# Kernel optimization log

Hardware: AMD Instinct MI355X
Metric: run time of the kernel (lower is better)

The kernel has to match this reference:

```python
import jax, jax.numpy as jnp
import numpy as np

CHEB_K = 3


def setup_inputs() -> dict:
    key = jax.random.key(0)
    k1, k2, k3 = jax.random.split(key, 3)
    B, N, C = 64, 2048, 64
    E, O = 16, 64
    x = jax.random.normal(k1, (B, N, C), dtype=jnp.float32)
    node_embeddings = jax.random.normal(k2, (N, E), dtype=jnp.float32)
    # xavier-uniform-like init for weights_pool (embed_dim, cheb_k, dim_in, dim_out)
    fan_in, fan_out = E * CHEB_K * C, O
    limit = float(np.sqrt(6.0 / (fan_in + fan_out)))
    weights_pool = jax.random.uniform(k3, (E, CHEB_K, C, O), dtype=jnp.float32,
                                      minval=-limit, maxval=limit)
    bias_pool = jnp.zeros((E, O), dtype=jnp.float32)
    return {"x": x, "node_embeddings": node_embeddings,
            "weights_pool": weights_pool, "bias_pool": bias_pool}


def reference(x, node_embeddings, weights_pool, bias_pool):
    N = node_embeddings.shape[0]
    # adaptive adjacency: softmax(relu(E E^T)) row-wise   [N, N]
    supports = jax.nn.softmax(jax.nn.relu(node_embeddings @ node_embeddings.T), axis=1)
    # Chebyshev recurrence: T0 = I, T1 = A, Tk = 2*A*T_{k-1} - T_{k-2}
    support_set = [jnp.eye(N, dtype=supports.dtype), supports]
    for _ in range(2, CHEB_K):
        support_set.append(2.0 * supports @ support_set[-1] - support_set[-2])
    supports_k = jnp.stack(support_set, axis=0)  # [K, N, N]
    # per-node dynamic weights / bias from pools
    weights = jnp.einsum('nd,dkio->nkio', node_embeddings, weights_pool)  # [N,K,C,O]
    bias = node_embeddings @ bias_pool                                    # [N,O]
    # graph conv: gather Chebyshev features then per-node grouped GEMM
    x_g = jnp.einsum('knm,bmc->bnkc', supports_k, x)       # [B,N,K,C]
    x_gconv = jnp.einsum('bnki,nkio->bno', x_g, weights) + bias  # [B,N,O]
    return x_gconv
```

## Files before the change

### kernel.cpp

```cpp
#include <hip/hip_runtime.h>
#include <hip/hip_bf16.h>

#define BB 64
#define NN 2048
#define CC 64
#define EE 16
#define OO 64
#define JJ 4096

typedef __attribute__((ext_vector_type(8))) short short8;
typedef __attribute__((ext_vector_type(4))) float f32x4;
typedef __attribute__((ext_vector_type(4))) unsigned short u16x4;
typedef __attribute__((ext_vector_type(8))) unsigned short u16x8;

__device__ __forceinline__ unsigned short f2bf(float f) {
  __hip_bfloat16 h = __float2bfloat16(f);
  return *reinterpret_cast<unsigned short*>(&h);
}
__device__ __forceinline__ float bf2f(unsigned short u) {
  unsigned int v = ((unsigned int)u) << 16;
  return *reinterpret_cast<float*>(&v);
}
__device__ __forceinline__ void gload16(const void* g, void* l) {
  __builtin_amdgcn_global_load_lds(
      (const __attribute__((address_space(1))) unsigned int*)g,
      (__attribute__((address_space(3))) unsigned int*)l, 16, 0, 0);
}

__global__ __launch_bounds__(256) void supports_kernel(
    const float* __restrict__ emb, unsigned short* __restrict__ A)
{
  int n = blockIdx.x;
  int tid = threadIdx.x;
  float en[EE];
#pragma unroll
  for (int d = 0; d < EE; ++d) en[d] = emb[n*EE + d];

  float logit[8];
  float lmax = 0.0f;
#pragma unroll
  for (int i = 0; i < 8; ++i) {
    int m = i*256 + tid;
    const float* em = emb + m*EE;
    float s = 0.f;
#pragma unroll
    for (int d = 0; d < EE; ++d) s = fmaf(en[d], em[d], s);
    s = fmaxf(s, 0.f);
    logit[i] = s;
    lmax = fmaxf(lmax, s);
  }
  __shared__ float red[256];
  red[tid] = lmax; __syncthreads();
  for (int s = 128; s > 0; s >>= 1) {
    if (tid < s) red[tid] = fmaxf(red[tid], red[tid+s]);
    __syncthreads();
  }
  lmax = red[0]; __syncthreads();
  float sum = 0.f;
#pragma unroll
  for (int i = 0; i < 8; ++i) {
    float e = __expf(logit[i]-lmax);
    logit[i] = e; sum += e;
  }
  red[tid] = sum; __syncthreads();
  for (int s = 128; s > 0; s >>= 1) {
    if (tid < s) red[tid] += red[tid+s];
    __syncthreads();
  }
  float inv = 1.f/red[0];
#pragma unroll
  for (int i = 0; i < 8; ++i) A[(size_t)n*NN + i*256 + tid] = f2bf(logit[i]*inv);
}

__global__ __launch_bounds__(256) void xpose_kernel(
    const float* __restrict__ x, unsigned short* __restrict__ Xt)
{
  int b = blockIdx.y;
  int n0 = blockIdx.x * 64;
  __shared__ float T[64][65];
  int tid = threadIdx.x;
  int r = tid >> 4, c4 = (tid & 15) * 4;
  const float* src = x + ((size_t)b*NN + n0)*64;
#pragma unroll
  for (int rr = r; rr < 64; rr += 16) {
    float4 v = *(const float4*)(src + rr*64 + c4);
    T[rr][c4] = v.x; T[rr][c4+1] = v.y; T[rr][c4+2] = v.z; T[rr][c4+3] = v.w;
  }
  __syncthreads();
  int c = tid >> 2, q0 = (tid & 3) * 16;
  unsigned short* dst = Xt + ((size_t)b*64 + c)*NN + n0 + q0;
  u16x8 o0, o1;
#pragma unroll
  for (int q = 0; q < 8; ++q) o0[q] = f2bf(T[q0+q][c]);
#pragma unroll
  for (int q = 0; q < 8; ++q) o1[q] = f2bf(T[q0+8+q][c]);
  *(u16x8*)(dst) = o0;
  *(u16x8*)(dst + 8) = o1;
}

__device__ __forceinline__ void stage_tile(
    const unsigned short* __restrict__ A, const unsigned short* __restrict__ Bt,
    unsigned short* as, unsigned short* bs,
    int m0, int j0, int k0, int wid, int lrow, int lu)
{
#pragma unroll
  for (int li = 0; li < 4; ++li) {
    int rb = wid*32 + li*8;
    int r = rb + lrow;
    int su = lu ^ (r & 7);
    gload16(A  + (size_t)(m0 + r)*2048 + k0 + su*8, as + rb*64);
    gload16(Bt + (size_t)(j0 + r)*2048 + k0 + su*8, bs + rb*64);
  }
}

__global__ __launch_bounds__(256) void gemm_bt_bf16(
    const unsigned short* __restrict__ A, const unsigned short* __restrict__ Bt,
    unsigned short* __restrict__ Crow, unsigned short* __restrict__ Ct, int writeT)
{
  __shared__ unsigned short As[2][128*64];
  __shared__ unsigned short Bs[2][128*64];
  int tid = threadIdx.x;
  int bid = blockIdx.x;
  int swz = (bid & 7) * 64 + (bid >> 3);
  int m0 = (swz >> 5) * 128, j0 = (swz & 31) * 128;
  int wid = tid >> 6, lane = tid & 63;
  int wm = wid >> 1, wn = wid & 1;
  int fr = lane & 15, kg = lane >> 4;
  int lrow = lane >> 3, lu = lane & 7;

  f32x4 acc[4][4];
#pragma unroll
  for (int i = 0; i < 4; ++i)
#pragma unroll
    for (int j = 0; j < 4; ++j) acc[i][j] = (f32x4){0.f,0.f,0.f,0.f};

  stage_tile(A, Bt, As[0], Bs[0], m0, j0, 0, wid, lrow, lu);

  int cur = 0;
#pragma unroll 2
  for (int k0 = 0; k0 < 2048; k0 += 64) {
    if (k0 + 64 < 2048) {
      stage_tile(A, Bt, As[cur^1], Bs[cur^1], m0, j0, k0 + 64, wid, lrow, lu);
      asm volatile("s_waitcnt vmcnt(8)" ::: "memory");
    } else {
      asm volatile("s_waitcnt vmcnt(0)" ::: "memory");
    }
    __builtin_amdgcn_s_barrier();
    asm volatile("" ::: "memory");

    const unsigned short* asb = As[cur];
    const unsigned short* bsb = Bs[cur];
#pragma unroll
    for (int ks = 0; ks < 2; ++ks) {
      short8 af[4], bv[4];
#pragma unroll
      for (int i = 0; i < 4; ++i) {
        int r = wm*64 + i*16 + fr;
        int u = ((ks << 2) | kg) ^ (r & 7);
        af[i] = *(const short8*)((const char*)asb + r*128 + u*16);
      }
#pragma unroll
      for (int j = 0; j < 4; ++j) {
        int r = wn*64 + j*16 + fr;
        int u = ((ks << 2) | kg) ^ (r & 7);
        bv[j] = *(const short8*)((const char*)bsb + r*128 + u*16);
      }
#pragma unroll
      for (int i = 0; i < 4; ++i)
#pragma unroll
        for (int j = 0; j < 4; ++j)
          acc[i][j] = __builtin_amdgcn_mfma_f32_16x16x32_bf16(af[i], bv[j], acc[i][j], 0, 0, 0);
    }
    asm volatile("" ::: "memory");
    __builtin_amdgcn_s_barrier();
    cur ^= 1;
  }

  int mrow4 = (lane >> 4) * 4;
#pragma unroll
  for (int i = 0; i < 4; ++i) {
    int mbase = m0 + wm*64 + i*16 + mrow4;
#pragma unroll
    for (int j = 0; j < 4; ++j) {
      int jcol = j0 + wn*64 + j*16 + fr;
      f32x4 v = acc[i][j];
      if (writeT) {
        u16x4 pk = { f2bf(v[0]), f2bf(v[1]), f2bf(v[2]), f2bf(v[3]) };
        *(u16x4*)(Ct + (size_t)jcol*2048 + mbase) = pk;
      }
      Crow[(size_t)(mbase+0)*4096 + jcol] = f2bf(v[0]);
      Crow[(size_t)(mbase+1)*4096 + jcol] = f2bf(v[1]);
      Crow[(size_t)(mbase+2)*4096 + jcol] = f2bf(v[2]);
      Crow[(size_t)(mbase+3)*4096 + jcol] = f2bf(v[3]);
    }
  }
}

__global__ __launch_bounds__(256) void wgen_kernel(
    const float* __restrict__ emb, const float* __restrict__ wp,
    unsigned short* __restrict__ wtg)
{
  __shared__ unsigned short Wlds[8][64*72];
  __shared__ float e_s[8][16];
  int tid = threadIdx.x;
  int g = blockIdx.x, r = blockIdx.y;
  int n0 = g*8;
  if (tid < 128) e_s[tid >> 4][tid & 15] = emb[n0*16 + tid];
  __syncthreads();
  int o = tid & 63, w = tid >> 6;
#pragma unroll 1
  for (int p = 0; p < 2; ++p) {
    int u = r*8 + p*4 + w;
    float acc[8][8];
#pragma unroll
    for (int n = 0; n < 8; ++n)
#pragma unroll
      for (int q = 0; q < 8; ++q) acc[n][q] = 0.f;
    const float* wpp = wp + u*512 + o;
#pragma unroll
    for (int d = 0; d < 16; ++d) {
      float wv[8];
#pragma unroll
      for (int q = 0; q < 8; ++q) wv[q] = wpp[d*12288 + q*64];
#pragma unroll
      for (int n = 0; n < 8; ++n) {
        float en = e_s[n][d];
#pragma unroll
        for (int q = 0; q < 8; ++q) acc[n][q] = fmaf(en, wv[q], acc[n][q]);
      }
    }
    int slot = (u & 7) ^ (o & 7);
#pragma unroll
    for (int n = 0; n < 8; ++n) {
      u16x8 pk;
#pragma unroll
      for (int q = 0; q < 8; ++q) pk[q] = f2bf(acc[n][q]);
      *(u16x8*)&Wlds[n][o*72 + slot*8] = pk;
    }
  }
  __syncthreads();
#pragma unroll
  for (int half = 0; half < 2; ++half) {
    int nd = half*4 + (tid >> 6);
    unsigned short* dst = wtg + (size_t)(n0+nd)*12288 + o*192 + r*64;
#pragma unroll
    for (int s = 0; s < 8; ++s)
      *(u16x8*)(dst + s*8) = *(const u16x8*)&Wlds[nd][o*72 + s*8];
  }
}

#define FNPB 4
__global__ __launch_bounds__(256) void final_mfma(
    const float* __restrict__ x, const float* __restrict__ emb,
    const float* __restrict__ bp, const unsigned short* __restrict__ wtg,
    const unsigned short* __restrict__ y1, const unsigned short* __restrict__ y2,
    float* __restrict__ out)
{
  __shared__ unsigned short Ws[2][12288];
  __shared__ unsigned short As[12288];
  int tid = threadIdx.x;
  int lane = tid & 63, wid = tid >> 6;
  int b = tid & 63;
  int fr = lane & 15, kg = lane >> 4;
  int o = wid*16 + fr;
  int nb = blockIdx.x * FNPB;

  float4 rx0[2][2], rx1[2][2];
  u16x8  ry1[2][2], ry2[2][2];

#pragma unroll
  for (int h = 0; h < 2; ++h) {
    int ul = wid + h*4;
    const float* xp = x + ((size_t)b*NN + nb)*64 + ul*8;
    rx0[0][h] = *(const float4*)xp;
    rx1[0][h] = *(const float4*)(xp + 4);
    ry1[0][h] = *(const u16x8*)(y1 + (size_t)nb*JJ + b*64 + ul*8);
    ry2[0][h] = *(const u16x8*)(y2 + (size_t)nb*JJ + b*64 + ul*8);
  }
#pragma unroll
  for (int t = 0; t < 6; ++t) {
    int base = wid*3072 + t*512;
    gload16(wtg + (size_t)nb*12288 + base + lane*8, &Ws[0][base]);
  }

#pragma unroll
  for (int i = 0; i < FNPB; ++i) {
    int n = nb + i;
    int cs = i & 1, ns = cs ^ 1;

#pragma unroll
    for (int h = 0; h < 2; ++h) {
      int ul = wid + h*4;
      float fx[8] = {rx0[cs][h].x, rx0[cs][h].y, rx0[cs][h].z, rx0[cs][h].w,
                     rx1[cs][h].x, rx1[cs][h].y, rx1[cs][h].z, rx1[cs][h].w};
      u16x8 v1 = ry1[cs][h], v2 = ry2[cs][h];
      u16x8 xb, t2;
#pragma unroll
      for (int q = 0; q < 8; ++q) {
        xb[q] = f2bf(fx[q]);
        t2[q] = f2bf(2.f*bf2f(v2[q]) - fx[q]);
      }
      int sw = ul ^ (b & 7);
      *(u16x8*)&As[b*192 + sw*8]      = xb;
      *(u16x8*)&As[b*192 + (8|sw)*8]  = v1;
      *(u16x8*)&As[b*192 + (16|sw)*8] = t2;
    }
    if (i + 1 < FNPB) {
#pragma unroll
      for (int h = 0; h < 2; ++h) {
        int ul = wid + h*4;
        const float* xp = x + ((size_t)b*NN + (n+1))*64 + ul*8;
        rx0[ns][h] = *(const float4*)xp;
        rx1[ns][h] = *(const float4*)(xp + 4);
        ry1[ns][h] = *(const u16x8*)(y1 + (size_t)(n+1)*JJ + b*64 + ul*8);
        ry2[ns][h] = *(const u16x8*)(y2 + (size_t)(n+1)*JJ + b*64 + ul*8);
      }
      asm volatile("s_waitcnt vmcnt(8)" ::: "memory");
    } else {
      asm volatile("s_waitcnt vmcnt(0)" ::: "memory");
    }
    asm volatile("s_waitcnt lgkmcnt(0)" ::: "memory");
    __builtin_amdgcn_s_barrier();
    asm volatile("" ::: "memory");

    float breg = 0.f;
#pragma unroll
    for (int d = 0; d < 16; ++d) breg = fmaf(emb[n*16 + d], bp[d*64 + o], breg);
    f32x4 acc[4];
#pragma unroll
    for (int k = 0; k < 4; ++k) acc[k] = (f32x4){breg, breg, breg, breg};

#pragma unroll
    for (int ks = 0; ks < 6; ++ks) {
      int u = ks*4 + kg;
      int ro = wid*16 + fr;
      int ub = (u & ~7) | ((u & 7) ^ (ro & 7));
      short8 bv = *(const short8*)&Ws[cs][ro*192 + ub*8];
#pragma unroll
      for (int k = 0; k < 4; ++k) {
        int ra = k*16 + fr;
        int ua = (u & ~7) | ((u & 7) ^ (ra & 7));
        short8 af = *(const short8*)&As[ra*192 + ua*8];
        acc[k] = __builtin_amdgcn_mfma_f32_16x16x32_bf16(af, bv, acc[k], 0, 0, 0);
      }
    }
    int mrow = (lane >> 4) * 4;
#pragma unroll
    for (int k = 0; k < 4; ++k) {
#pragma unroll
      for (int rr = 0; rr < 4; ++rr) {
        int brow = k*16 + mrow + rr;
        out[((size_t)brow*NN + n)*64 + o] = acc[k][rr];
      }
    }
    if (i + 1 < FNPB) {
#pragma unroll
      for (int t = 0; t < 6; ++t) {
        int base = wid*3072 + t*512;
        gload16(wtg + (size_t)(n+1)*12288 + base + lane*8, &Ws[ns][base]);
      }
    }
    asm volatile("" ::: "memory");
    __builtin_amdgcn_s_barrier();
  }
}

extern "C" void kernel_launch(void* const* d_in, const int* in_sizes, int n_in,
                              void* d_out, int out_size, void* d_ws, size_t ws_size,
                              hipStream_t stream) {
  const float* x   = (const float*)d_in[0];
  const float* emb = (const float*)d_in[1];
  const float* wp  = (const float*)d_in[2];
  const float* bp  = (const float*)d_in[3];
  float* out = (float*)d_out;

  unsigned short* Ab  = (unsigned short*)d_ws;
  unsigned short* Y1b = Ab  + (size_t)NN*NN;
  unsigned short* Y2b = Y1b + (size_t)NN*JJ;
  unsigned short* region = Y2b + (size_t)NN*JJ;
  unsigned short* Xt  = region;
  unsigned short* Y1T = region + (size_t)JJ*NN;
  unsigned short* Wtg = region;

  supports_kernel<<<NN, 256, 0, stream>>>(emb, Ab);
  xpose_kernel<<<dim3(32, 64), 256, 0, stream>>>(x, Xt);
  dim3 g(512);
  gemm_bt_bf16<<<g, 256, 0, stream>>>(Ab, Xt,  Y1b, Y1T, 1);
  gemm_bt_bf16<<<g, 256, 0, stream>>>(Ab, Y1T, Y2b, nullptr, 0);
  wgen_kernel<<<dim3(256, 3), 256, 0, stream>>>(emb, wp, Wtg);
  final_mfma<<<NN/FNPB, 256, 0, stream>>>(x, emb, bp, Wtg, Y1b, Y2b, out);
}
```

Before: 181.8 us.

## Rework bf16 GEMM into 8-wave 128x256 tile with triple-buffered phased pipeline

Replaces the 256-thread 128x128 double-buffered GEMM with a 512-thread kernel that computes 128x256 output tiles using three LDS buffers. Global-to-LDS staging is split into chunks interleaved with four MFMA sub-phases per K-tile, separated by barriers, and s_setprio raises priority around MFMA bursts. The aim is to hide global load latency and improve operand reuse, with the grid halved to 256 blocks. The cost is more LDS per block, more barriers, and fewer blocks in flight for the GPU's CUs.

After: 209.6 us. +15.3%, slower.

```diff
diff --git a/kernel.cpp b/kernel.cpp
--- a/kernel.cpp
+++ b/kernel.cpp
@@ -98,33 +98,21 @@
   *(u16x8*)(dst + 8) = o1;
 }
 
-__device__ __forceinline__ void stage_tile(
-    const unsigned short* __restrict__ A, const unsigned short* __restrict__ Bt,
-    unsigned short* as, unsigned short* bs,
-    int m0, int j0, int k0, int wid, int lrow, int lu)
-{
-#pragma unroll
-  for (int li = 0; li < 4; ++li) {
-    int rb = wid*32 + li*8;
-    int r = rb + lrow;
-    int su = lu ^ (r & 7);
-    gload16(A  + (size_t)(m0 + r)*2048 + k0 + su*8, as + rb*64);
-    gload16(Bt + (size_t)(j0 + r)*2048 + k0 + su*8, bs + rb*64);
-  }
-}
-
-__global__ __launch_bounds__(256) void gemm_bt_bf16(
+#define BAR() do { asm volatile("" ::: "memory"); __builtin_amdgcn_s_barrier(); \
+                   asm volatile("" ::: "memory"); } while(0)
+
+__global__ __launch_bounds__(512) void gemm_bt_8p(
     const unsigned short* __restrict__ A, const unsigned short* __restrict__ Bt,
     unsigned short* __restrict__ Crow, unsigned short* __restrict__ Ct, int writeT)
 {
-  __shared__ unsigned short As[2][128*64];
-  __shared__ unsigned short Bs[2][128*64];
+  __shared__ unsigned short As[3][128*64];
+  __shared__ unsigned short Bs[3][256*64];
   int tid = threadIdx.x;
   int bid = blockIdx.x;
-  int swz = (bid & 7) * 64 + (bid >> 3);
-  int m0 = (swz >> 5) * 128, j0 = (swz & 31) * 128;
+  int swz = (bid & 7) * 32 + (bid >> 3);
+  int m0 = (swz >> 4) * 128, j0 = (swz & 15) * 256;
   int wid = tid >> 6, lane = tid & 63;
-  int wm = wid >> 1, wn = wid & 1;
+  int wm = wid >> 2, wn = wid & 3;
   int fr = lane & 15, kg = lane >> 4;
   int lrow = lane >> 3, lu = lane & 7;
 
@@ -134,47 +122,74 @@
 #pragma unroll
     for (int j = 0; j < 4; ++j) acc[i][j] = (f32x4){0.f,0.f,0.f,0.f};
 
-  stage_tile(A, Bt, As[0], Bs[0], m0, j0, 0, wid, lrow, lu);
-
-  int cur = 0;
-#pragma unroll 2
-  for (int k0 = 0; k0 < 2048; k0 += 64) {
-    if (k0 + 64 < 2048) {
-      stage_tile(A, Bt, As[cur^1], Bs[cur^1], m0, j0, k0 + 64, wid, lrow, lu);
-      asm volatile("s_waitcnt vmcnt(8)" ::: "memory");
-    } else {
-      asm volatile("s_waitcnt vmcnt(0)" ::: "memory");
-    }
-    __builtin_amdgcn_s_barrier();
-    asm volatile("" ::: "memory");
-
-    const unsigned short* asb = As[cur];
-    const unsigned short* bsb = Bs[cur];
-#pragma unroll
-    for (int ks = 0; ks < 2; ++ks) {
-      short8 af[4], bv[4];
-#pragma unroll
-      for (int i = 0; i < 4; ++i) {
-        int r = wm*64 + i*16 + fr;
+  auto stageA = [&](int bW, int k0, int c) {
+    int rb = wid*16 + c*8;
+    gload16(A + (size_t)(m0 + rb + lrow)*2048 + k0 + (lu ^ lrow)*8, &As[bW][rb*64]);
+  };
+  auto stageB = [&](int bW, int k0, int c) {
+    int rb = wid*32 + c*8;
+    gload16(Bt + (size_t)(j0 + rb + lrow)*2048 + k0 + (lu ^ lrow)*8, &Bs[bW][rb*64]);
+  };
+  auto phase = [&](int bR, int q) {
+    int qi = q >> 1, qj = q & 1;
+    short8 af[2][2], bv[2][2];
+#pragma unroll
+    for (int di = 0; di < 2; ++di)
+#pragma unroll
+      for (int ks = 0; ks < 2; ++ks) {
+        int r = wm*64 + (qi*2 + di)*16 + fr;
         int u = ((ks << 2) | kg) ^ (r & 7);
-        af[i] = *(const short8*)((const char*)asb + r*128 + u*16);
-      }
-#pragma unroll
-      for (int j = 0; j < 4; ++j) {
-        int r = wn*64 + j*16 + fr;
+        af[di][ks] = *(const short8*)((const char*)&As[bR][0] + r*128 + u*16);
+      }
+#pragma unroll
+    for (int dj = 0; dj < 2; ++dj)
+#pragma unroll
+      for (int ks = 0; ks < 2; ++ks) {
+        int r = wn*64 + (qj*2 + dj)*16 + fr;
         int u = ((ks << 2) | kg) ^ (r & 7);
-        bv[j] = *(const short8*)((const char*)bsb + r*128 + u*16);
-      }
-#pragma unroll
-      for (int i = 0; i < 4; ++i)
-#pragma unroll
-        for (int j = 0; j < 4; ++j)
-          acc[i][j] = __builtin_amdgcn_mfma_f32_16x16x32_bf16(af[i], bv[j], acc[i][j], 0, 0, 0);
-    }
-    asm volatile("" ::: "memory");
-    __builtin_amdgcn_s_barrier();
-    cur ^= 1;
-  }
+        bv[dj][ks] = *(const short8*)((const char*)&Bs[bR][0] + r*128 + u*16);
+      }
+    __builtin_amdgcn_s_setprio(1);
+#pragma unroll
+    for (int di = 0; di < 2; ++di)
+#pragma unroll
+      for (int dj = 0; dj < 2; ++dj)
+#pragma unroll
+        for (int ks = 0; ks < 2; ++ks)
+          acc[qi*2+di][qj*2+dj] = __builtin_amdgcn_mfma_f32_16x16x32_bf16(
+              af[di][ks], bv[dj][ks], acc[qi*2+di][qj*2+dj], 0, 0, 0);
+    __builtin_amdgcn_s_setprio(0);
+  };
+
+#define TILE(bR, bW, kS, DOST, EW) do {                                   \
+    if (DOST) { stageA(bW, kS, 0); stageB(bW, kS, 0); }                   \
+    phase(bR, 0); BAR();                                                  \
+    if (DOST) { stageA(bW, kS, 1); stageB(bW, kS, 1); }                   \
+    phase(bR, 1); BAR();                                                  \
+    if (DOST) { stageB(bW, kS, 2); stageB(bW, kS, 3); }                   \
+    phase(bR, 2); BAR();                                                  \
+    phase(bR, 3);                                                         \
+    if ((EW) == 6) asm volatile("s_waitcnt vmcnt(6)" ::: "memory");       \
+    else if ((EW) == 0) asm volatile("s_waitcnt vmcnt(0)" ::: "memory");  \
+    if ((EW) >= 0) BAR();                                                 \
+  } while(0)
+
+  stageA(0, 0, 0); stageA(0, 0, 1);
+  stageB(0, 0, 0); stageB(0, 0, 1); stageB(0, 0, 2); stageB(0, 0, 3);
+  stageA(1, 64, 0); stageA(1, 64, 1);
+  stageB(1, 64, 0); stageB(1, 64, 1); stageB(1, 64, 2); stageB(1, 64, 3);
+  asm volatile("s_waitcnt vmcnt(6)" ::: "memory");
+  BAR();
+
+  for (int tg = 0; tg < 10; ++tg) {
+    int kb = tg * 192;
+    TILE(0, 2, kb + 128, 1, 6);
+    TILE(1, 0, kb + 192, 1, 6);
+    TILE(2, 1, kb + 256, 1, 6);
+  }
+  TILE(0, 2, 0, 0, 0);
+  TILE(1, 0, 0, 0, -1);
+#undef TILE
 
   int mrow4 = (lane >> 4) * 4;
 #pragma unroll
@@ -384,9 +399,8 @@
 
   supports_kernel<<<NN, 256, 0, stream>>>(emb, Ab);
   xpose_kernel<<<dim3(32, 64), 256, 0, stream>>>(x, Xt);
-  dim3 g(512);
-  gemm_bt_bf16<<<g, 256, 0, stream>>>(Ab, Xt,  Y1b, Y1T, 1);
-  gemm_bt_bf16<<<g, 256, 0, stream>>>(Ab, Y1T, Y2b, nullptr, 0);
+  gemm_bt_8p<<<256, 512, 0, stream>>>(Ab, Xt,  Y1b, Y1T, 1);
+  gemm_bt_8p<<<256, 512, 0, stream>>>(Ab, Y1T, Y2b, nullptr, 0);
   wgen_kernel<<<dim3(256, 3), 256, 0, stream>>>(emb, wp, Wtg);
   final_mfma<<<NN/FNPB, 256, 0, stream>>>(x, emb, bp, Wtg, Y1b, Y2b, out);
 }
```

## Fold Chebyshev T2 combination into generated weights and simplify final kernel

Applied to the files above, without the earlier changes.

The T2 = 2*A*Y1 - X combination is moved into the weight generator: the k=0 weights become W0-W2 and the k=2 weights are scaled by 2. The final kernel can then load raw Y1/Y2 rows straight into LDS with async global-to-LDS loads instead of doing elementwise fixup in registers. The GEMM epilogue writes Y rows with an XOR swizzle that matches the LDS layout the final kernel reads. The final kernel now handles one node per block with no double-buffered pipeline, which removes VALU conversion work but gives up the cross-node prefetch overlap.

Result: slower. 247.4 us (+36.1%).

```diff
diff --git a/kernel.cpp b/kernel.cpp
--- a/kernel.cpp
+++ b/kernel.cpp
@@ -188,10 +188,11 @@
         u16x4 pk = { f2bf(v[0]), f2bf(v[1]), f2bf(v[2]), f2bf(v[3]) };
         *(u16x4*)(Ct + (size_t)jcol*2048 + mbase) = pk;
       }
-      Crow[(size_t)(mbase+0)*4096 + jcol] = f2bf(v[0]);
-      Crow[(size_t)(mbase+1)*4096 + jcol] = f2bf(v[1]);
-      Crow[(size_t)(mbase+2)*4096 + jcol] = f2bf(v[2]);
-      Crow[(size_t)(mbase+3)*4096 + jcol] = f2bf(v[3]);
+      int jc2 = jcol ^ ((jcol & 0x1C0) >> 3);
+      Crow[(size_t)(mbase+0)*4096 + jc2] = f2bf(v[0]);
+      Crow[(size_t)(mbase+1)*4096 + jc2] = f2bf(v[1]);
+      Crow[(size_t)(mbase+2)*4096 + jc2] = f2bf(v[2]);
+      Crow[(size_t)(mbase+3)*4096 + jc2] = f2bf(v[3]);
     }
   }
 }
@@ -208,6 +209,7 @@
   if (tid < 128) e_s[tid >> 4][tid & 15] = emb[n0*16 + tid];
   __syncthreads();
   int o = tid & 63, w = tid >> 6;
+  float kscale = (r == 2) ? 2.f : 1.f;
 #pragma unroll 1
   for (int p = 0; p < 2; ++p) {
     int u = r*8 + p*4 + w;
@@ -221,7 +223,11 @@
     for (int d = 0; d < 16; ++d) {
       float wv[8];
 #pragma unroll
-      for (int q = 0; q < 8; ++q) wv[q] = wpp[d*12288 + q*64];
+      for (int q = 0; q < 8; ++q) {
+        float v = wpp[d*12288 + q*64];
+        if (r == 0) v -= wpp[d*12288 + q*64 + 8192];
+        wv[q] = v;
+      }
 #pragma unroll
       for (int n = 0; n < 8; ++n) {
         float en = e_s[n][d];
@@ -234,7 +240,7 @@
     for (int n = 0; n < 8; ++n) {
       u16x8 pk;
 #pragma unroll
-      for (int q = 0; q < 8; ++q) pk[q] = f2bf(acc[n][q]);
+      for (int q = 0; q < 8; ++q) pk[q] = f2bf(acc[n][q] * kscale);
       *(u16x8*)&Wlds[n][o*72 + slot*8] = pk;
     }
   }
@@ -249,119 +255,73 @@
   }
 }
 
-#define FNPB 4
 __global__ __launch_bounds__(256) void final_mfma(
     const float* __restrict__ x, const float* __restrict__ emb,
     const float* __restrict__ bp, const unsigned short* __restrict__ wtg,
     const unsigned short* __restrict__ y1, const unsigned short* __restrict__ y2,
     float* __restrict__ out)
 {
-  __shared__ unsigned short Ws[2][12288];
-  __shared__ unsigned short As[12288];
+  __shared__ unsigned short As[3*4096];
+  __shared__ unsigned short Ws[12288];
   int tid = threadIdx.x;
   int lane = tid & 63, wid = tid >> 6;
-  int b = tid & 63;
   int fr = lane & 15, kg = lane >> 4;
   int o = wid*16 + fr;
-  int nb = blockIdx.x * FNPB;
-
-  float4 rx0[2][2], rx1[2][2];
-  u16x8  ry1[2][2], ry2[2][2];
-
-#pragma unroll
-  for (int h = 0; h < 2; ++h) {
-    int ul = wid + h*4;
-    const float* xp = x + ((size_t)b*NN + nb)*64 + ul*8;
-    rx0[0][h] = *(const float4*)xp;
-    rx1[0][h] = *(const float4*)(xp + 4);
-    ry1[0][h] = *(const u16x8*)(y1 + (size_t)nb*JJ + b*64 + ul*8);
-    ry2[0][h] = *(const u16x8*)(y2 + (size_t)nb*JJ + b*64 + ul*8);
-  }
+  int n = blockIdx.x;
+
 #pragma unroll
   for (int t = 0; t < 6; ++t) {
     int base = wid*3072 + t*512;
-    gload16(wtg + (size_t)nb*12288 + base + lane*8, &Ws[0][base]);
-  }
-
-#pragma unroll
-  for (int i = 0; i < FNPB; ++i) {
-    int n = nb + i;
-    int cs = i & 1, ns = cs ^ 1;
-
-#pragma unroll
-    for (int h = 0; h < 2; ++h) {
-      int ul = wid + h*4;
-      float fx[8] = {rx0[cs][h].x, rx0[cs][h].y, rx0[cs][h].z, rx0[cs][h].w,
-                     rx1[cs][h].x, rx1[cs][h].y, rx1[cs][h].z, rx1[cs][h].w};
-      u16x8 v1 = ry1[cs][h], v2 = ry2[cs][h];
-      u16x8 xb, t2;
-#pragma unroll
-      for (int q = 0; q < 8; ++q) {
-        xb[q] = f2bf(fx[q]);
-        t2[q] = f2bf(2.f*bf2f(v2[q]) - fx[q]);
-      }
-      int sw = ul ^ (b & 7);
-      *(u16x8*)&As[b*192 + sw*8]      = xb;
-      *(u16x8*)&As[b*192 + (8|sw)*8]  = v1;
-      *(u16x8*)&As[b*192 + (16|sw)*8] = t2;
-    }
-    if (i + 1 < FNPB) {
-#pragma unroll
-      for (int h = 0; h < 2; ++h) {
-        int ul = wid + h*4;
-        const float* xp = x + ((size_t)b*NN + (n+1))*64 + ul*8;
-        rx0[ns][h] = *(const float4*)xp;
-        rx1[ns][h] = *(const float4*)(xp + 4);
-        ry1[ns][h] = *(const u16x8*)(y1 + (size_t)(n+1)*JJ + b*64 + ul*8);
-        ry2[ns][h] = *(const u16x8*)(y2 + (size_t)(n+1)*JJ + b*64 + ul*8);
-      }
-      asm volatile("s_waitcnt vmcnt(8)" ::: "memory");
-    } else {
-      asm volatile("s_waitcnt vmcnt(0)" ::: "memory");
-    }
-    asm volatile("s_waitcnt lgkmcnt(0)" ::: "memory");
-    __builtin_amdgcn_s_barrier();
-    asm volatile("" ::: "memory");
-
-    float breg = 0.f;
-#pragma unroll
-    for (int d = 0; d < 16; ++d) breg = fmaf(emb[n*16 + d], bp[d*64 + o], breg);
-    f32x4 acc[4];
-#pragma unroll
-    for (int k = 0; k < 4; ++k) acc[k] = (f32x4){breg, breg, breg, breg};
-
-#pragma unroll
-    for (int ks = 0; ks < 6; ++ks) {
-      int u = ks*4 + kg;
-      int ro = wid*16 + fr;
-      int ub = (u & ~7) | ((u & 7) ^ (ro & 7));
-      short8 bv = *(const short8*)&Ws[cs][ro*192 + ub*8];
-#pragma unroll
-      for (int k = 0; k < 4; ++k) {
-        int ra = k*16 + fr;
-        int ua = (u & ~7) | ((u & 7) ^ (ra & 7));
-        short8 af = *(const short8*)&As[ra*192 + ua*8];
-        acc[k] = __builtin_amdgcn_mfma_f32_16x16x32_bf16(af, bv, acc[k], 0, 0, 0);
-      }
-    }
-    int mrow = (lane >> 4) * 4;
+    gload16(wtg + (size_t)n*12288 + base + lane*8, &Ws[base]);
+  }
+#pragma unroll
+  for (int t = 0; t < 2; ++t) {
+    int base = wid*512 + t*2048;
+    gload16(y1 + (size_t)n*JJ + base + lane*8, &As[4096 + base]);
+    gload16(y2 + (size_t)n*JJ + base + lane*8, &As[8192 + base]);
+  }
+  int b = tid & 63, q = tid >> 6;
+#pragma unroll
+  for (int h = 0; h < 2; ++h) {
+    int ul = q + h*4;
+    const float* xp = x + ((size_t)b*NN + n)*64 + ul*8;
+    float4 v0 = *(const float4*)xp;
+    float4 v1 = *(const float4*)(xp + 4);
+    float fx[8] = {v0.x,v0.y,v0.z,v0.w,v1.x,v1.y,v1.z,v1.w};
+    u16x8 xb;
+#pragma unroll
+    for (int e = 0; e < 8; ++e) xb[e] = f2bf(fx[e]);
+    *(u16x8*)&As[b*64 + (ul ^ (b & 7))*8] = xb;
+  }
+  __syncthreads();
+
+  float breg = 0.f;
+#pragma unroll
+  for (int d = 0; d < 16; ++d) breg = fmaf(emb[n*16 + d], bp[d*64 + o], breg);
+  f32x4 acc[4];
+#pragma unroll
+  for (int k = 0; k < 4; ++k) acc[k] = (f32x4){breg, breg, breg, breg};
+
+#pragma unroll
+  for (int ks = 0; ks < 6; ++ks) {
+    int u = ks*4 + kg;
+    int p = u >> 3, uu = u & 7;
+    short8 bv = *(const short8*)&Ws[o*192 + ((u & ~7) | (uu ^ (o & 7)))*8];
 #pragma unroll
     for (int k = 0; k < 4; ++k) {
-#pragma unroll
-      for (int rr = 0; rr < 4; ++rr) {
-        int brow = k*16 + mrow + rr;
-        out[((size_t)brow*NN + n)*64 + o] = acc[k][rr];
-      }
-    }
-    if (i + 1 < FNPB) {
-#pragma unroll
-      for (int t = 0; t < 6; ++t) {
-        int base = wid*3072 + t*512;
-        gload16(wtg + (size_t)(n+1)*12288 + base + lane*8, &Ws[ns][base]);
-      }
-    }
-    asm volatile("" ::: "memory");
-    __builtin_amdgcn_s_barrier();
+      int ra = k*16 + fr;
+      short8 af = *(const short8*)&As[p*4096 + ra*64 + (uu ^ (ra & 7))*8];
+      acc[k] = __builtin_amdgcn_mfma_f32_16x16x32_bf16(af, bv, acc[k], 0, 0, 0);
+    }
+  }
+  int mrow = (lane >> 4) * 4;
+#pragma unroll
+  for (int k = 0; k < 4; ++k) {
+#pragma unroll
+    for (int rr = 0; rr < 4; ++rr) {
+      int brow = k*16 + mrow + rr;
+      out[((size_t)brow*NN + n)*64 + o] = acc[k][rr];
+    }
   }
 }
 
@@ -388,5 +348,5 @@
   gemm_bt_bf16<<<g, 256, 0, stream>>>(Ab, Xt,  Y1b, Y1T, 1);
   gemm_bt_bf16<<<g, 256, 0, stream>>>(Ab, Y1T, Y2b, nullptr, 0);
   wgen_kernel<<<dim3(256, 3), 256, 0, stream>>>(emb, wp, Wtg);
-  final_mfma<<<NN/FNPB, 256, 0, stream>>>(x, emb, bp, Wtg, Y1b, Y2b, out);
-}
+  final_mfma<<<NN, 256, 0, stream>>>(x, emb, bp, Wtg, Y1b, Y2b, out);
+}
```
